# Kernel optimization log

Measured on AMD Instinct MI355X. Metric: run time of the kernel, lower is better.

Reference implementation:

```python
import jax, jax.numpy as jnp
import numpy as np

D_MODEL = 512
N_HEADS = 8
HEAD_DIM = D_MODEL // N_HEADS  # 64


def setup_inputs() -> dict:
    key = jax.random.key(0)
    ks = jax.random.split(key, 12)
    B, SQ, SK = 4, 2048, 2048
    s = 1.0 / np.sqrt(D_MODEL)
    return {
        "query": jax.random.normal(ks[0], (B, SQ, D_MODEL), jnp.float32),
        "key": jax.random.normal(ks[1], (B, SK, D_MODEL), jnp.float32),
        "value": jax.random.normal(ks[2], (B, SK, D_MODEL), jnp.float32),
        "Wq": jax.random.normal(ks[3], (D_MODEL, D_MODEL), jnp.float32) * s,
        "bq": jnp.zeros((D_MODEL,), jnp.float32),
        "Wk": jax.random.normal(ks[4], (D_MODEL, D_MODEL), jnp.float32) * s,
        "bk": jnp.zeros((D_MODEL,), jnp.float32),
        "Wv": jax.random.normal(ks[5], (D_MODEL, D_MODEL), jnp.float32) * s,
        "bv": jnp.zeros((D_MODEL,), jnp.float32),
        "Wo": jax.random.normal(ks[6], (D_MODEL, D_MODEL), jnp.float32) * s,
        "bo": jnp.zeros((D_MODEL,), jnp.float32),
    }


def reference(query, key, value, Wq, bq, Wk, bk, Wv, bv, Wo, bo):
    B, SQ, _ = query.shape
    SK = key.shape[1]
    # QKV projections
    Q = query @ Wq.T + bq  # [B,SQ,D]
    K = key @ Wk.T + bk    # [B,SK,D]
    V = value @ Wv.T + bv  # [B,SK,D]
    # split heads -> [B,H,S,hd]
    Q = Q.reshape(B, SQ, N_HEADS, HEAD_DIM).transpose(0, 2, 1, 3)
    K = K.reshape(B, SK, N_HEADS, HEAD_DIM).transpose(0, 2, 1, 3)
    V = V.reshape(B, SK, N_HEADS, HEAD_DIM).transpose(0, 2, 1, 3)
    scale = jnp.sqrt(jnp.float32(HEAD_DIM))
    scores = jnp.einsum('bhqd,bhkd->bhqk', Q, K) / scale  # [B,H,SQ,SK]
    attn = jax.nn.softmax(scores, axis=-1)  # dropout p=0 (eval)
    ctx = jnp.einsum('bhqk,bhkd->bhqd', attn, V)
    ctx = ctx.transpose(0, 2, 1, 3).reshape(B, SQ, D_MODEL)
    # exact (erf) GELU as in torch F.gelu default
    out = jax.nn.gelu(ctx, approximate=False) @ Wo.T + bo
    return out
```

## Files before the change

kernel.cpp:

```cpp
#include <hip/hip_runtime.h>
#include <hip/hip_bf16.h>

#define D_MODEL 512
#define N_HEADS 8
#define HEAD_DIM 64
#define BATCH 4
#define SEQ 2048

typedef _Float16 f16;
typedef _Float16 f16x8 __attribute__((ext_vector_type(8)));
typedef _Float16 f16x4 __attribute__((ext_vector_type(4)));
typedef float f32x4 __attribute__((ext_vector_type(4)));
typedef unsigned int u32x4 __attribute__((ext_vector_type(4)));

#define MFMA16(a, b, c) __builtin_amdgcn_mfma_f32_16x16x32_f16((a), (b), (c), 0, 0, 0)

#define GLOAD_LDS16(src, dst)                                                   \
    __builtin_amdgcn_global_load_lds(                                           \
        (const __attribute__((address_space(1))) void*)(src),                   \
        (__attribute__((address_space(3))) void*)(dst), 16, 0, 0)

#if __has_builtin(__builtin_amdgcn_exp2f)
#define EXP2(x) __builtin_amdgcn_exp2f(x)
#else
#define EXP2(x) __expf((x) * 0.6931471805599453f)
#endif

#define QSCALE 0.18033688011112042f
#define OFF2 8.656170245333781f

__global__ __launch_bounds__(256) void wsplit(
    const float* __restrict__ w0, const float* __restrict__ w1,
    const float* __restrict__ w2, const float* __restrict__ w3,
    f16* __restrict__ h0, f16* __restrict__ h1,
    f16* __restrict__ h2, f16* __restrict__ h3)
{
    const int j = blockIdx.y;
    const float* s = (j == 0) ? w0 : (j == 1) ? w1 : (j == 2) ? w2 : w3;
    f16* dh = (j == 0) ? h0 : (j == 1) ? h1 : (j == 2) ? h2 : h3;
    const int n4 = (D_MODEL * D_MODEL) >> 2;
    for (int i = blockIdx.x * 256 + threadIdx.x; i < n4; i += gridDim.x * 256) {
        float4 x = ((const float4*)s)[i];
        f16x4 hv = {(f16)x.x, (f16)x.y, (f16)x.z, (f16)x.w};
        ((f16x4*)dh)[i] = hv;
    }
}

__global__ __launch_bounds__(256, 3) void proj_mfma(
    const float* __restrict__ Xq, const float* __restrict__ Xk,
    const float* __restrict__ Xv,
    const f16* __restrict__ Wqh, const f16* __restrict__ Wkh,
    const f16* __restrict__ Wvh,
    const float* __restrict__ bq, const float* __restrict__ bk,
    const float* __restrict__ bv,
    f16* __restrict__ Qh, f16* __restrict__ Kh, f16* __restrict__ Vt)
{
    __shared__ f16 ldsA[128 * 64];
    __shared__ f16 ldsW[128 * 64];

    const int z = blockIdx.z;
    const float* X = (z == 0) ? Xq : (z == 1) ? Xk : Xv;
    const f16* Wh = (z == 0) ? Wqh : (z == 1) ? Wkh : Wvh;
    const float* bias = (z == 0) ? bq : (z == 1) ? bk : bv;

    const int m0 = blockIdx.x * 128;
    const int n0 = blockIdx.y * 128;

    const int tid = threadIdx.x;
    const int w = tid >> 6, l = tid & 63;
    const int lp = l >> 4, lq = l & 15;
    const int wm = w >> 1, wn = w & 1;

    f32x4 acc[4][4] = {};

    for (int kt = 0; kt < D_MODEL; kt += 64) {
        __syncthreads();
        float4 av[4][2];
        int arow[4], aslot[4];
#pragma unroll
        for (int j = 0; j < 4; ++j) {
            const int chunk = j * 256 + tid;
            arow[j] = chunk >> 3;
            aslot[j] = chunk & 7;
            const float* sp = X + (size_t)(m0 + arow[j]) * D_MODEL + kt + aslot[j] * 8;
            av[j][0] = *(const float4*)sp;
            av[j][1] = *(const float4*)(sp + 4);
        }
#pragma unroll
        for (int j = 0; j < 4; ++j) {
            const int cb = j * 256 + w * 64;
            const int chunk = cb + l;
            const int row = chunk >> 3;
            const int slot = (chunk & 7) ^ (row & 7);
            GLOAD_LDS16(Wh + (size_t)(n0 + row) * D_MODEL + kt + slot * 8,
                        ldsW + cb * 8);
        }
#pragma unroll
        for (int j = 0; j < 4; ++j) {
            f16x8 hv;
            hv[0] = (f16)av[j][0].x; hv[1] = (f16)av[j][0].y;
            hv[2] = (f16)av[j][0].z; hv[3] = (f16)av[j][0].w;
            hv[4] = (f16)av[j][1].x; hv[5] = (f16)av[j][1].y;
            hv[6] = (f16)av[j][1].z; hv[7] = (f16)av[j][1].w;
            *(f16x8*)(ldsA + arow[j] * 64 + ((aslot[j] ^ (arow[j] & 7)) << 3)) = hv;
        }
        __syncthreads();

        f16x8 af[4][2];
#pragma unroll
        for (int mt = 0; mt < 4; ++mt) {
            const int R = wm * 64 + mt * 16 + lq;
#pragma unroll
            for (int s = 0; s < 2; ++s)
                af[mt][s] = *(const f16x8*)(ldsA + R * 64 + (((s * 4 + lp) ^ (R & 7)) << 3));
        }
        __builtin_amdgcn_s_setprio(1);
#pragma unroll
        for (int nt = 0; nt < 4; ++nt) {
            const int R = wn * 64 + nt * 16 + lq;
            f16x8 b0 = *(const f16x8*)(ldsW + R * 64 + (((0 + lp) ^ (R & 7)) << 3));
            f16x8 b1 = *(const f16x8*)(ldsW + R * 64 + (((4 + lp) ^ (R & 7)) << 3));
#pragma unroll
            for (int mt = 0; mt < 4; ++mt) {
                acc[mt][nt] = MFMA16(af[mt][0], b0, acc[mt][nt]);
                acc[mt][nt] = MFMA16(af[mt][1], b1, acc[mt][nt]);
            }
        }
        __builtin_amdgcn_s_setprio(0);
    }

    const int m_base = m0 + wm * 64;
    const int n_base = n0 + wn * 64;
    const int b = m0 / SEQ;
    const int h = n_base >> 6;
    const size_t bh_ = (size_t)b * N_HEADS + h;

    if (z == 0) {
#pragma unroll
        for (int nt = 0; nt < 4; ++nt) {
            const int n = n_base + nt * 16 + lq;
            const float bn = bias[n];
            const int d = n & 63;
#pragma unroll
            for (int mt = 0; mt < 4; ++mt) {
#pragma unroll
                for (int r = 0; r < 4; ++r) {
                    const int s = (m_base + mt * 16 + lp * 4 + r) & (SEQ - 1);
                    Qh[(bh_ * SEQ + s) * 64 + d] = (f16)((acc[mt][nt][r] + bn) * QSCALE);
                }
            }
        }
    } else if (z == 1) {
#pragma unroll
        for (int nt = 0; nt < 4; ++nt) {
            const int n = n_base + nt * 16 + lq;
            const float bn = bias[n];
            const int d = n & 63;
#pragma unroll
            for (int mt = 0; mt < 4; ++mt) {
#pragma unroll
                for (int r = 0; r < 4; ++r) {
                    const int s = (m_base + mt * 16 + lp * 4 + r) & (SEQ - 1);
                    Kh[(bh_ * SEQ + s) * 64 + d] = (f16)(acc[mt][nt][r] + bn);
                }
            }
        }
    } else {
#pragma unroll
        for (int nt = 0; nt < 4; ++nt) {
            const int n = n_base + nt * 16 + lq;
            const float bn = bias[n];
            const int d = n & 63;
#pragma unroll
            for (int mt = 0; mt < 4; ++mt) {
                const int s0 = (m_base + mt * 16 + lp * 4) & (SEQ - 1);
                f16x4 col;
#pragma unroll
                for (int r = 0; r < 4; ++r)
                    col[r] = (f16)(acc[mt][nt][r] + bn);
                *(f16x4*)(Vt + (bh_ * 64 + d) * SEQ + s0) = col;
            }
        }
    }
}

__global__ __launch_bounds__(256, 4) void out_mfma(
    const f16* __restrict__ Gh, const f16* __restrict__ Woh,
    const float* __restrict__ bo, float* __restrict__ Out)
{
    __shared__ f16 ldsA[64 * 64];
    __shared__ f16 ldsW[128 * 64];

    const int m0 = blockIdx.x * 64;
    const int n0 = blockIdx.y * 128;

    const int tid = threadIdx.x;
    const int w = tid >> 6, l = tid & 63;
    const int lp = l >> 4, lq = l & 15;
    const int wm = w >> 1, wn = w & 1;

    f32x4 acc[2][4] = {};

    for (int kt = 0; kt < D_MODEL; kt += 64) {
        __syncthreads();
#pragma unroll
        for (int j = 0; j < 2; ++j) {
            const int cb = j * 256 + w * 64;
            const int chunk = cb + l;
            const int row = chunk >> 3;
            const int slot = (chunk & 7) ^ (row & 7);
            GLOAD_LDS16(Gh + (size_t)(m0 + row) * D_MODEL + kt + slot * 8,
                        ldsA + cb * 8);
        }
#pragma unroll
        for (int j = 0; j < 4; ++j) {
            const int cb = j * 256 + w * 64;
            const int chunk = cb + l;
            const int row = chunk >> 3;
            const int slot = (chunk & 7) ^ (row & 7);
            GLOAD_LDS16(Woh + (size_t)(n0 + row) * D_MODEL + kt + slot * 8,
                        ldsW + cb * 8);
        }
        __syncthreads();

        f16x8 af[2][2];
#pragma unroll
        for (int mt = 0; mt < 2; ++mt) {
            const int R = wm * 32 + mt * 16 + lq;
#pragma unroll
            for (int s = 0; s < 2; ++s)
                af[mt][s] = *(const f16x8*)(ldsA + R * 64 + (((s * 4 + lp) ^ (R & 7)) << 3));
        }
        __builtin_amdgcn_s_setprio(1);
#pragma unroll
        for (int nt = 0; nt < 4; ++nt) {
            const int R = wn * 64 + nt * 16 + lq;
            f16x8 b0 = *(const f16x8*)(ldsW + R * 64 + (((0 + lp) ^ (R & 7)) << 3));
            f16x8 b1 = *(const f16x8*)(ldsW + R * 64 + (((4 + lp) ^ (R & 7)) << 3));
#pragma unroll
            for (int mt = 0; mt < 2; ++mt) {
                acc[mt][nt] = MFMA16(af[mt][0], b0, acc[mt][nt]);
                acc[mt][nt] = MFMA16(af[mt][1], b1, acc[mt][nt]);
            }
        }
        __builtin_amdgcn_s_setprio(0);
    }

#pragma unroll
    for (int nt = 0; nt < 4; ++nt) {
        const int n = n0 + wn * 64 + nt * 16 + lq;
        const float bn = bo[n];
#pragma unroll
        for (int mt = 0; mt < 2; ++mt) {
#pragma unroll
            for (int r = 0; r < 4; ++r) {
                const int m = m0 + wm * 32 + mt * 16 + lp * 4 + r;
                Out[(size_t)m * D_MODEL + n] = acc[mt][nt][r] + bn;
            }
        }
    }
}

__global__ __launch_bounds__(256, 2) void flash_mfma(
    const f16* __restrict__ Qh, const f16* __restrict__ Kh,
    const f16* __restrict__ Vt, f16* __restrict__ Gh)
{
    __shared__ f16 KV[2][2][4096];

    const int tid = threadIdx.x;
    const int w  = tid >> 6;
    const int l  = tid & 63;
    const int lp = l >> 4;
    const int lq = l & 15;

    const int id = blockIdx.x;
    const int work = (id & 7) * 64 + (id >> 3);
    const int bh = work >> 4;
    const int b  = bh >> 3, h = bh & 7;
    const int q0 = (work & 15) * 128 + w * 32;

    f16x8 qf[2][2];
#pragma unroll
    for (int sub = 0; sub < 2; ++sub)
#pragma unroll
        for (int s = 0; s < 2; ++s)
            qf[sub][s] = *(const f16x8*)(Qh + ((size_t)bh * SEQ + q0 + sub * 16 + lq) * 64
                                          + s * 32 + lp * 8);

    f16x8 ones;
#pragma unroll
    for (int i = 0; i < 8; ++i) ones[i] = (f16)1.f;

    f32x4 o[2][4];
#pragma unroll
    for (int sub = 0; sub < 2; ++sub)
#pragma unroll
        for (int c = 0; c < 4; ++c) o[sub][c] = (f32x4){0.f, 0.f, 0.f, 0.f};
    f32x4 lf[2] = {(f32x4){0.f, 0.f, 0.f, 0.f}, (f32x4){0.f, 0.f, 0.f, 0.f}};

    auto STAGE = [&](int k0, int bf) {
#pragma unroll
        for (int j = 0; j < 4; ++j) {
            const int gi = w + 4 * j;
            const int tset = gi >> 3;
            const int t = gi & 7;
            const int lrow = t * 8 + (l >> 3);
            const int slot = (l & 7) ^ (lrow & 7);
            if (tset == 0)
                GLOAD_LDS16(Kh + ((size_t)bh * SEQ + k0 + lrow) * 64 + slot * 8,
                            &KV[bf][0][t * 512]);
            else
                GLOAD_LDS16(Vt + ((size_t)bh * 64 + lrow) * SEQ + k0 + slot * 8,
                            &KV[bf][1][t * 512]);
        }
    };

    auto QKT = [&](int bf, f32x4 (&st)[2][4], f16x8 (&vbr)[2][4]) {
        const f16* Kt_ = &KV[bf][0][0];
        const f16* Vt_ = &KV[bf][1][0];
#pragma unroll
        for (int sub = 0; sub < 2; ++sub)
#pragma unroll
            for (int c = 0; c < 4; ++c)
                st[sub][c] = (f32x4){-OFF2, -OFF2, -OFF2, -OFF2};
        __builtin_amdgcn_s_setprio(1);
#pragma unroll
        for (int mt = 0; mt < 4; ++mt) {
            const int krow = mt * 16 + lq;
#pragma unroll
            for (int s = 0; s < 2; ++s) {
                const int byteoff = krow * 128 + (((4 * s + lp) ^ (krow & 7)) << 4);
                f16x8 ah = *(const f16x8*)((const char*)Kt_ + byteoff);
#pragma unroll
                for (int sub = 0; sub < 2; ++sub)
                    st[sub][mt] = MFMA16(ah, qf[sub][s], st[sub][mt]);
            }
        }
        __builtin_amdgcn_s_setprio(0);
#pragma unroll
        for (int s = 0; s < 2; ++s)
#pragma unroll
            for (int nt = 0; nt < 4; ++nt) {
                const int d = nt * 16 + lq;
                const int byteoff = d * 128 + (((4 * s + lp) ^ (d & 7)) << 4);
                vbr[s][nt] = *(const f16x8*)((const char*)Vt_ + byteoff);
            }
    };

    auto SMPV = [&](f32x4 (&st)[2][4], f16x8 (&vbr)[2][4]) {
        f16x8 pa[2][2];
#pragma unroll
        for (int sub = 0; sub < 2; ++sub) {
            unsigned int pk0[4], pk1[4];
#pragma unroll
            for (int mt = 0; mt < 4; ++mt) {
                float e0 = EXP2(st[sub][mt][0]);
                float e1 = EXP2(st[sub][mt][1]);
                float e2 = EXP2(st[sub][mt][2]);
                float e3 = EXP2(st[sub][mt][3]);
                pk0[mt] = __builtin_bit_cast(unsigned int,
                              __builtin_amdgcn_cvt_pkrtz(e0, e1));
                pk1[mt] = __builtin_bit_cast(unsigned int,
                              __builtin_amdgcn_cvt_pkrtz(e2, e3));
            }
#pragma unroll
            for (int s = 0; s < 2; ++s) {
                unsigned int x0 = pk0[2 * s], y0 = pk0[2 * s + 1];
                unsigned int x1 = pk1[2 * s], y1 = pk1[2 * s + 1];
                asm("v_permlane32_swap_b32 %0, %1" : "+v"(x0), "+v"(y0));
                asm("v_permlane16_swap_b32 %0, %1" : "+v"(x0), "+v"(y0));
                asm("v_permlane32_swap_b32 %0, %1" : "+v"(x1), "+v"(y1));
                asm("v_permlane16_swap_b32 %0, %1" : "+v"(x1), "+v"(y1));
                u32x4 t4 = {x0, x1, y0, y1};
                pa[sub][s] = __builtin_bit_cast(f16x8, t4);
            }
        }
        __builtin_amdgcn_s_setprio(1);
#pragma unroll
        for (int s = 0; s < 2; ++s) {
#pragma unroll
            for (int sub = 0; sub < 2; ++sub) {
                lf[sub] = MFMA16(pa[sub][s], ones, lf[sub]);
#pragma unroll
                for (int nt = 0; nt < 4; ++nt)
                    o[sub][nt] = MFMA16(pa[sub][s], vbr[s][nt], o[sub][nt]);
            }
        }
        __builtin_amdgcn_s_setprio(0);
    };

    f32x4 stA[2][4], stB[2][4];
    f16x8 vbrA[2][4], vbrB[2][4];

    STAGE(0, 0);
    asm volatile("s_waitcnt vmcnt(0)" ::: "memory");
    __builtin_amdgcn_s_barrier();
    STAGE(64, 1);
    __builtin_amdgcn_sched_barrier(0);
    QKT(0, stA, vbrA);

#pragma unroll 1
    for (int tt = 0; tt < 15; ++tt) {
        const int t1 = 2 * tt + 1;
        asm volatile("s_waitcnt vmcnt(0)" ::: "memory");
        __builtin_amdgcn_s_barrier();
        STAGE((t1 + 1) * 64, 0);
        __builtin_amdgcn_sched_barrier(0);
        QKT(1, stB, vbrB);
        SMPV(stA, vbrA);

        asm volatile("s_waitcnt vmcnt(0)" ::: "memory");
        __builtin_amdgcn_s_barrier();
        STAGE((t1 + 2) * 64, 1);
        __builtin_amdgcn_sched_barrier(0);
        QKT(0, stA, vbrA);
        SMPV(stB, vbrB);
    }

    asm volatile("s_waitcnt vmcnt(0)" ::: "memory");
    __builtin_amdgcn_s_barrier();
    __builtin_amdgcn_sched_barrier(0);
    QKT(1, stB, vbrB);
    SMPV(stA, vbrA);
    SMPV(stB, vbrB);

#pragma unroll
    for (int sub = 0; sub < 2; ++sub) {
#pragma unroll
        for (int j = 0; j < 4; ++j) {
            const float inv = 1.f / lf[sub][j];
            const int row = q0 + sub * 16 + lp * 4 + j;
#pragma unroll
            for (int nt = 0; nt < 4; ++nt) {
                float x = o[sub][nt][j] * inv;
                float g = 0.5f * x * (1.f + erff(x * 0.70710678118654752f));
                Gh[((size_t)(b * SEQ + row)) * D_MODEL + h * 64 + nt * 16 + lq] = (f16)g;
            }
        }
    }
}

extern "C" void kernel_launch(void* const* d_in, const int* in_sizes, int n_in,
                              void* d_out, int out_size, void* d_ws, size_t ws_size,
                              hipStream_t stream)
{
    const float* query = (const float*)d_in[0];
    const float* key   = (const float*)d_in[1];
    const float* value = (const float*)d_in[2];
    const float* Wq = (const float*)d_in[3];
    const float* bq = (const float*)d_in[4];
    const float* Wk = (const float*)d_in[5];
    const float* bk = (const float*)d_in[6];
    const float* Wv = (const float*)d_in[7];
    const float* bv = (const float*)d_in[8];
    const float* Wo = (const float*)d_in[9];
    const float* bo = (const float*)d_in[10];

    char* ws = (char*)d_ws;
    const size_t MB = 1024 * 1024;
    const size_t KB = 1024;
    f16* Qh = (f16*)(ws + 0 * MB);
    f16* Kh = (f16*)(ws + 8 * MB);
    f16* Vt = (f16*)(ws + 16 * MB);
    f16* Gh = (f16*)(ws + 24 * MB);
    f16* Wqh = (f16*)(ws + 32 * MB);
    f16* Wkh = (f16*)(ws + 32 * MB + 512 * KB);
    f16* Wvh = (f16*)(ws + 33 * MB);
    f16* Woh = (f16*)(ws + 33 * MB + 512 * KB);

    wsplit<<<dim3(64, 4), 256, 0, stream>>>(Wq, Wk, Wv, Wo, Wqh, Wkh, Wvh, Woh);

    proj_mfma<<<dim3(BATCH * SEQ / 128, D_MODEL / 128, 3), 256, 0, stream>>>(
        query, key, value, Wqh, Wkh, Wvh, bq, bk, bv, Qh, Kh, Vt);

    flash_mfma<<<dim3(512), 256, 0, stream>>>(Qh, Kh, Vt, Gh);

    out_mfma<<<dim3(BATCH * SEQ / 64, D_MODEL / 128), 256, 0, stream>>>(
        Gh, Woh, bo, (float*)d_out);
}
```

Measured before the change: 85.51 us.

## Widen projection tiles to 128x256 and precompute flash LDS/global addressing

```diff
diff --git a/kernel.cpp b/kernel.cpp
--- a/kernel.cpp
+++ b/kernel.cpp
@@ -46,7 +46,7 @@
     }
 }
 
-__global__ __launch_bounds__(256, 3) void proj_mfma(
+__global__ __launch_bounds__(512, 4) void proj_mfma(
     const float* __restrict__ Xq, const float* __restrict__ Xk,
     const float* __restrict__ Xv,
     const f16* __restrict__ Wqh, const f16* __restrict__ Wkh,
@@ -56,7 +56,7 @@
     f16* __restrict__ Qh, f16* __restrict__ Kh, f16* __restrict__ Vt)
 {
     __shared__ f16 ldsA[128 * 64];
-    __shared__ f16 ldsW[128 * 64];
+    __shared__ f16 ldsW[256 * 64];
 
     const int z = blockIdx.z;
     const float* X = (z == 0) ? Xq : (z == 1) ? Xk : Xv;
@@ -64,22 +64,22 @@
     const float* bias = (z == 0) ? bq : (z == 1) ? bk : bv;
 
     const int m0 = blockIdx.x * 128;
-    const int n0 = blockIdx.y * 128;
+    const int n0 = blockIdx.y * 256;
 
     const int tid = threadIdx.x;
     const int w = tid >> 6, l = tid & 63;
     const int lp = l >> 4, lq = l & 15;
-    const int wm = w >> 1, wn = w & 1;
+    const int wm = w >> 2, wn = w & 3;
 
     f32x4 acc[4][4] = {};
 
     for (int kt = 0; kt < D_MODEL; kt += 64) {
         __syncthreads();
-        float4 av[4][2];
-        int arow[4], aslot[4];
-#pragma unroll
-        for (int j = 0; j < 4; ++j) {
-            const int chunk = j * 256 + tid;
+        float4 av[2][2];
+        int arow[2], aslot[2];
+#pragma unroll
+        for (int j = 0; j < 2; ++j) {
+            const int chunk = j * 512 + tid;
             arow[j] = chunk >> 3;
             aslot[j] = chunk & 7;
             const float* sp = X + (size_t)(m0 + arow[j]) * D_MODEL + kt + aslot[j] * 8;
@@ -88,7 +88,7 @@
         }
 #pragma unroll
         for (int j = 0; j < 4; ++j) {
-            const int cb = j * 256 + w * 64;
+            const int cb = j * 512 + w * 64;
             const int chunk = cb + l;
             const int row = chunk >> 3;
             const int slot = (chunk & 7) ^ (row & 7);
@@ -96,7 +96,7 @@
                         ldsW + cb * 8);
         }
 #pragma unroll
-        for (int j = 0; j < 4; ++j) {
+        for (int j = 0; j < 2; ++j) {
             f16x8 hv;
             hv[0] = (f16)av[j][0].x; hv[1] = (f16)av[j][0].y;
             hv[2] = (f16)av[j][0].z; hv[3] = (f16)av[j][0].w;
@@ -290,6 +290,7 @@
     f16x8 ones;
 #pragma unroll
     for (int i = 0; i < 8; ++i) ones[i] = (f16)1.f;
+    const f32x4 OFFI = (f32x4){-OFF2, -OFF2, -OFF2, -OFF2};
 
     f32x4 o[2][4];
 #pragma unroll
@@ -298,53 +299,58 @@
         for (int c = 0; c < 4; ++c) o[sub][c] = (f32x4){0.f, 0.f, 0.f, 0.f};
     f32x4 lf[2] = {(f32x4){0.f, 0.f, 0.f, 0.f}, (f32x4){0.f, 0.f, 0.f, 0.f}};
 
-    auto STAGE = [&](int k0, int bf) {
-#pragma unroll
-        for (int j = 0; j < 4; ++j) {
-            const int gi = w + 4 * j;
-            const int tset = gi >> 3;
-            const int t = gi & 7;
-            const int lrow = t * 8 + (l >> 3);
-            const int slot = (l & 7) ^ (lrow & 7);
-            if (tset == 0)
-                GLOAD_LDS16(Kh + ((size_t)bh * SEQ + k0 + lrow) * 64 + slot * 8,
-                            &KV[bf][0][t * 512]);
-            else
-                GLOAD_LDS16(Vt + ((size_t)bh * 64 + lrow) * SEQ + k0 + slot * 8,
-                            &KV[bf][1][t * 512]);
-        }
+    int koff[4][2], voff[2][4];
+#pragma unroll
+    for (int mt = 0; mt < 4; ++mt) {
+        const int krow = mt * 16 + lq;
+#pragma unroll
+        for (int s = 0; s < 2; ++s)
+            koff[mt][s] = krow * 128 + (((4 * s + lp) ^ (krow & 7)) << 4);
+    }
+#pragma unroll
+    for (int s = 0; s < 2; ++s)
+#pragma unroll
+        for (int nt = 0; nt < 4; ++nt) {
+            const int d = nt * 16 + lq;
+            voff[s][nt] = d * 128 + (((4 * s + lp) ^ (d & 7)) << 4);
+        }
+
+    const int lr0 = w * 8 + (l >> 3);
+    const int lr1 = (w + 4) * 8 + (l >> 3);
+    const f16* kp0 = Kh + ((size_t)bh * SEQ + lr0) * 64 + (((l & 7) ^ (lr0 & 7)) << 3);
+    const f16* kp1 = Kh + ((size_t)bh * SEQ + lr1) * 64 + (((l & 7) ^ (lr1 & 7)) << 3);
+    const f16* vp0 = Vt + ((size_t)bh * 64 + lr0) * SEQ + (((l & 7) ^ (lr0 & 7)) << 3);
+    const f16* vp1 = Vt + ((size_t)bh * 64 + lr1) * SEQ + (((l & 7) ^ (lr1 & 7)) << 3);
+
+    auto STAGE = [&](int bf) {
+        GLOAD_LDS16(kp0, &KV[bf][0][w * 512]);
+        GLOAD_LDS16(kp1, &KV[bf][0][(w + 4) * 512]);
+        GLOAD_LDS16(vp0, &KV[bf][1][w * 512]);
+        GLOAD_LDS16(vp1, &KV[bf][1][(w + 4) * 512]);
+        kp0 += 64 * 64; kp1 += 64 * 64;
+        vp0 += 64;      vp1 += 64;
     };
 
     auto QKT = [&](int bf, f32x4 (&st)[2][4], f16x8 (&vbr)[2][4]) {
-        const f16* Kt_ = &KV[bf][0][0];
-        const f16* Vt_ = &KV[bf][1][0];
-#pragma unroll
-        for (int sub = 0; sub < 2; ++sub)
-#pragma unroll
-            for (int c = 0; c < 4; ++c)
-                st[sub][c] = (f32x4){-OFF2, -OFF2, -OFF2, -OFF2};
+        const char* Kt_ = (const char*)&KV[bf][0][0];
+        const char* Vt_ = (const char*)&KV[bf][1][0];
         __builtin_amdgcn_s_setprio(1);
 #pragma unroll
         for (int mt = 0; mt < 4; ++mt) {
-            const int krow = mt * 16 + lq;
-#pragma unroll
-            for (int s = 0; s < 2; ++s) {
-                const int byteoff = krow * 128 + (((4 * s + lp) ^ (krow & 7)) << 4);
-                f16x8 ah = *(const f16x8*)((const char*)Kt_ + byteoff);
-#pragma unroll
-                for (int sub = 0; sub < 2; ++sub)
-                    st[sub][mt] = MFMA16(ah, qf[sub][s], st[sub][mt]);
+            f16x8 ah0 = *(const f16x8*)(Kt_ + koff[mt][0]);
+            f16x8 ah1 = *(const f16x8*)(Kt_ + koff[mt][1]);
+#pragma unroll
+            for (int sub = 0; sub < 2; ++sub) {
+                st[sub][mt] = MFMA16(ah0, qf[sub][0], OFFI);
+                st[sub][mt] = MFMA16(ah1, qf[sub][1], st[sub][mt]);
             }
         }
         __builtin_amdgcn_s_setprio(0);
 #pragma unroll
         for (int s = 0; s < 2; ++s)
 #pragma unroll
-            for (int nt = 0; nt < 4; ++nt) {
-                const int d = nt * 16 + lq;
-                const int byteoff = d * 128 + (((4 * s + lp) ^ (d & 7)) << 4);
-                vbr[s][nt] = *(const f16x8*)((const char*)Vt_ + byteoff);
-            }
+            for (int nt = 0; nt < 4; ++nt)
+                vbr[s][nt] = *(const f16x8*)(Vt_ + voff[s][nt]);
     };
 
     auto SMPV = [&](f32x4 (&st)[2][4], f16x8 (&vbr)[2][4]) {
@@ -392,26 +398,25 @@
     f32x4 stA[2][4], stB[2][4];
     f16x8 vbrA[2][4], vbrB[2][4];
 
-    STAGE(0, 0);
+    STAGE(0);
     asm volatile("s_waitcnt vmcnt(0)" ::: "memory");
     __builtin_amdgcn_s_barrier();
-    STAGE(64, 1);
+    STAGE(1);
     __builtin_amdgcn_sched_barrier(0);
     QKT(0, stA, vbrA);
 
 #pragma unroll 1
     for (int tt = 0; tt < 15; ++tt) {
-        const int t1 = 2 * tt + 1;
         asm volatile("s_waitcnt vmcnt(0)" ::: "memory");
         __builtin_amdgcn_s_barrier();
-        STAGE((t1 + 1) * 64, 0);
+        STAGE(0);
         __builtin_amdgcn_sched_barrier(0);
         QKT(1, stB, vbrB);
         SMPV(stA, vbrA);
 
         asm volatile("s_waitcnt vmcnt(0)" ::: "memory");
         __builtin_amdgcn_s_barrier();
-        STAGE((t1 + 2) * 64, 1);
+        STAGE(1);
         __builtin_amdgcn_sched_barrier(0);
         QKT(0, stA, vbrA);
         SMPV(stB, vbrB);
@@ -470,7 +475,7 @@
 
     wsplit<<<dim3(64, 4), 256, 0, stream>>>(Wq, Wk, Wv, Wo, Wqh, Wkh, Wvh, Woh);
 
-    proj_mfma<<<dim3(BATCH * SEQ / 128, D_MODEL / 128, 3), 256, 0, stream>>>(
+    proj_mfma<<<dim3(BATCH * SEQ / 128, D_MODEL / 256, 3), 512, 0, stream>>>(
         query, key, value, Wqh, Wkh, Wvh, bq, bk, bv, Qh, Kh, Vt);
 
     flash_mfma<<<dim3(512), 256, 0, stream>>>(Qh, Kh, Vt, Gh);
```

Measured after the change: 92.25 us. 1.08x slower.
